# Kernel tuning notes

Hardware: AMD Instinct MI355X
Metric: run time of the kernel (lower is better)

Reference implementation:

```python
import jax, jax.numpy as jnp
import numpy as np

B, S, H, I, E, K = 2, 1024, 768, 1536, 8, 2
CAPACITY_FACTOR = 1.5
ROUTING_TEMP = 1.0
LB_WEIGHT = 0.001


def setup_inputs() -> dict:
    key = jax.random.key(0)
    k_x, k_g, k_w1, k_w3, k_w2 = jax.random.split(key, 5)
    std = 0.02
    return {
        "x": jax.random.normal(k_x, (B, S, H), dtype=jnp.float32),
        "w_gate": jax.random.normal(k_g, (H, E), dtype=jnp.float32) * 0.02,
        "w1": jax.random.normal(k_w1, (E, H, I), dtype=jnp.float32) * std,
        "w3": jax.random.normal(k_w3, (E, H, I), dtype=jnp.float32) * std,
        "w2": jax.random.normal(k_w2, (E, I, H), dtype=jnp.float32) * (std / np.sqrt(2 * 12)),
    }


def _moe_forward(x, w_gate, w1, w3, w2):
    Bb, Ss, Hh = x.shape
    T = Bb * Ss
    xf = x.reshape(T, Hh)

    # --- routing ---
    gate_logits = (xf @ w_gate) / ROUTING_TEMP          # [T, E]
    gate_probs = jax.nn.softmax(gate_logits, axis=-1)   # [T, E]
    topk_probs, topk_idx = jax.lax.top_k(gate_probs, K)  # [T, K]
    topk_probs = topk_probs / (topk_probs.sum(-1, keepdims=True) + 1e-8)

    # --- capacity dropping (per-k slot, token order, like the torch loop) ---
    capacity = max(8, int((T * K // E) * CAPACITY_FACTOR))
    onehot = (topk_idx[:, :, None] == jnp.arange(E)[None, None, :])  # [T, K, E] bool
    ranks = jnp.cumsum(onehot.astype(jnp.int32), axis=0)             # position of token in expert queue
    keep = onehot & (ranks <= capacity)                               # [T, K, E]

    # combine weight per (token, expert): sum over k of kept, clamped routing prob
    w_clamped = jnp.clip(topk_probs, 1e-8, 10.0)                      # [T, K]
    combine = jnp.einsum("tk,tke->te", w_clamped, keep.astype(xf.dtype))  # [T, E]

    # --- dense per-expert SwiGLU (reference form of masked dispatch) ---
    g = jnp.einsum("th,ehi->tei", xf, w1)   # [T, E, I]
    u = jnp.einsum("th,ehi->tei", xf, w3)   # [T, E, I]
    h = jax.nn.silu(g) * u                    # [T, E, I]
    y = jnp.einsum("tei,eih->teh", h, w2)   # [T, E, H]
    out = jnp.einsum("te,teh->th", combine, y).reshape(Bb, Ss, Hh)

    # --- load balancing loss ---
    expert_counts = keep.sum(axis=(0, 1)).astype(jnp.float32)         # [E]
    dropped = (onehot.sum() - keep.sum()).astype(jnp.float32)
    expert_usage = jax.lax.stop_gradient(expert_counts) / float(max(T * K, 1))
    gate_importance = gate_probs.mean(axis=0)                          # [E]
    aux = jnp.sum(expert_usage * gate_importance) * E
    aux = aux + jnp.where(dropped > 0, dropped / float(max(T, 1)) * 0.1, 0.0)
    aux = jnp.minimum(aux, 1.0) * LB_WEIGHT
    return out, aux


def reference(x, w_gate, w1, w3, w2):
    return _moe_forward(x, w_gate, w1, w3, w2)
```

## Files before the change

kernel.cpp:

```cpp
#include <hip/hip_runtime.h>
#include <math.h>

#define T_TOK 2048
#define HD 768
#define ID 1536
#define NE 8
#define CAP 768
#define TK 4096
#define RT 12
#define NB1 24
#define KC1 24
#define NB2 12
#define KC2 48
#define W2BLK 576

typedef __bf16 bf16_t;
typedef __bf16 bf16x8 __attribute__((ext_vector_type(8)));
typedef __bf16 bf16x4 __attribute__((ext_vector_type(4)));
typedef float floatx4 __attribute__((ext_vector_type(4)));

__device__ __forceinline__ void gld16(const bf16_t* g, bf16_t* l) {
  __builtin_amdgcn_global_load_lds(
      (__attribute__((address_space(1))) void*)(g),
      (__attribute__((address_space(3))) void*)(l),
      16, 0, 0);
}

__device__ __forceinline__ void repack_unit256(const float* __restrict__ src,
                                               bf16_t* __restrict__ dst, int C,
                                               int kc0, int tid) {
  int n = tid >> 2, p4 = tid & 3;
  int c8 = p4 ^ ((n >> 1) & 3);
  const float* sp0 = src + n + (size_t)(kc0 * 32 + c8 * 8) * C;
  bf16_t* dp = dst + (size_t)kc0 * 2048 + tid * 8;
#pragma unroll 2
  for (int t = 0; t < 8; ++t) {
    const float* sp = sp0 + (size_t)t * 32 * C;
    float v[8];
#pragma unroll
    for (int j = 0; j < 8; ++j) v[j] = sp[(size_t)j * C];
    bf16x8 o;
#pragma unroll
    for (int j = 0; j < 8; ++j) o[j] = (bf16_t)v[j];
    *(bf16x8*)(dp + t * 2048) = o;
  }
}

__device__ __forceinline__ void repack_unit1024(const float* __restrict__ src,
                                                bf16_t* __restrict__ dst, int C,
                                                int kc0, int tid1024) {
  int tid = tid1024 & 255;
  int tq = tid1024 >> 8;
  int n = tid >> 2, p4 = tid & 3;
  int c8 = p4 ^ ((n >> 1) & 3);
  const float* sp0 = src + n + (size_t)(kc0 * 32 + c8 * 8) * C;
  bf16_t* dp = dst + (size_t)kc0 * 2048 + tid * 8;
#pragma unroll
  for (int tt = 0; tt < 2; ++tt) {
    int t = tq * 2 + tt;
    const float* sp = sp0 + (size_t)t * 32 * C;
    float v[8];
#pragma unroll
    for (int j = 0; j < 8; ++j) v[j] = sp[(size_t)j * C];
    bf16x8 o;
#pragma unroll
    for (int j = 0; j < 8; ++j) o[j] = (bf16_t)v[j];
    *(bf16x8*)(dp + t * 2048) = o;
  }
}

__global__ void k_route(const float* __restrict__ x, const float* __restrict__ wg,
                        bf16_t* __restrict__ xbf, int2* __restrict__ idx2,
                        float2* __restrict__ wc2, float* __restrict__ probs8) {
  int b = blockIdx.x;
  int tid = threadIdx.x;
  int t = b * 4 + (tid >> 6);
  int lane = tid & 63;
  const float* xr = x + (size_t)t * HD;
  int off = lane * 12;
  float4 a = *(const float4*)(xr + off);
  float4 bv = *(const float4*)(xr + off + 4);
  float4 c = *(const float4*)(xr + off + 8);
  float xv[12] = {a.x, a.y, a.z, a.w, bv.x, bv.y, bv.z, bv.w, c.x, c.y, c.z, c.w};
  bf16x4 s0, s1, s2;
#pragma unroll
  for (int j = 0; j < 4; ++j) { s0[j] = (bf16_t)xv[j]; s1[j] = (bf16_t)xv[4 + j]; s2[j] = (bf16_t)xv[8 + j]; }
  bf16_t* xo = xbf + (size_t)t * HD + off;
  *(bf16x4*)xo = s0; *(bf16x4*)(xo + 4) = s1; *(bf16x4*)(xo + 8) = s2;

  float acc[8] = {0, 0, 0, 0, 0, 0, 0, 0};
#pragma unroll
  for (int jj = 0; jj < 12; ++jj) {
    const float4* wr = (const float4*)(wg + (size_t)(off + jj) * 8);
    float4 w0 = wr[0], w1v = wr[1];
    float v = xv[jj];
    acc[0] += v * w0.x; acc[1] += v * w0.y; acc[2] += v * w0.z; acc[3] += v * w0.w;
    acc[4] += v * w1v.x; acc[5] += v * w1v.y; acc[6] += v * w1v.z; acc[7] += v * w1v.w;
  }
#pragma unroll
  for (int e = 0; e < 8; ++e) {
    float v = acc[e];
    for (int s = 1; s < 64; s <<= 1) v += __shfl_xor(v, s, 64);
    acc[e] = v;
  }
  float mx = acc[0];
#pragma unroll
  for (int e = 1; e < 8; ++e) mx = fmaxf(mx, acc[e]);
  float p[8], sum = 0.f;
#pragma unroll
  for (int e = 0; e < 8; ++e) { p[e] = __expf(acc[e] - mx); sum += p[e]; }
#pragma unroll
  for (int e = 0; e < 8; ++e) p[e] /= sum;
  if (lane == 0) {
    float4 P0 = make_float4(p[0], p[1], p[2], p[3]);
    float4 P1 = make_float4(p[4], p[5], p[6], p[7]);
    *(float4*)&probs8[t * 8] = P0;
    *(float4*)&probs8[t * 8 + 4] = P1;
    int e0 = 0;
#pragma unroll
    for (int e = 1; e < 8; ++e) if (p[e] > p[e0]) e0 = e;
    int e1 = (e0 == 0) ? 1 : 0;
#pragma unroll
    for (int e = 0; e < 8; ++e) if (e != e0 && p[e] > p[e1]) e1 = e;
    float denom = p[e0] + p[e1] + 1e-8f;
    float w0c = fminf(fmaxf(p[e0] / denom, 1e-8f), 10.f);
    float w1c = fminf(fmaxf(p[e1] / denom, 1e-8f), 10.f);
    idx2[t] = make_int2(e0, e1);
    wc2[t] = make_float2(w0c, w1c);
  }
}

__global__ void k_scan(const int2* __restrict__ idx2, const float2* __restrict__ wc2,
                       const float* __restrict__ probs8,
                       const float* __restrict__ w1, const float* __restrict__ w3,
                       bf16_t* __restrict__ w1b, bf16_t* __restrict__ w3b,
                       int* __restrict__ tok_of_row, int2* __restrict__ rows2,
                       int2* __restrict__ cnt_start, float* __restrict__ aux_out) {
  if (blockIdx.x > 0) {
    int rb = blockIdx.x - 1;
    int m = rb >= 576;
    int r3 = m ? rb - 576 : rb;
    int pan = r3 / 3;
    int kc0 = (r3 - pan * 3) * 8;
    int e = pan & 7, nb = pan >> 3;
    const float* src = (m ? w3 : w1) + (size_t)e * HD * ID + nb * 64;
    bf16_t* dst = (m ? w3b : w1b) + (size_t)(e * NB1 + nb) * (KC1 * 2048);
    repack_unit1024(src, dst, ID, kc0, threadIdx.x);
    return;
  }
  __shared__ int2 sIdx[2048];
  __shared__ int sTot[16];
  __shared__ int sPos[8];
  __shared__ float sImp[16][8];
  int tid = threadIdx.x;
  sIdx[tid] = idx2[tid]; sIdx[tid + 1024] = idx2[tid + 1024];
  rows2[tid] = make_int2(-1, -1); rows2[tid + 1024] = make_int2(-1, -1);
  const float4* pp = (const float4*)probs8;
  float4 u0 = pp[tid * 4], u1 = pp[tid * 4 + 1], u2 = pp[tid * 4 + 2], u3 = pp[tid * 4 + 3];
  float im[8] = {u0.x + u2.x, u0.y + u2.y, u0.z + u2.z, u0.w + u2.w,
                 u1.x + u3.x, u1.y + u3.y, u1.z + u3.z, u1.w + u3.w};
#pragma unroll
  for (int e = 0; e < 8; ++e) {
    float v = im[e];
    for (int d = 1; d < 64; d <<= 1) v += __shfl_xor(v, d, 64);
    im[e] = v;
  }
  int w = tid >> 6, lane = tid & 63;
  if (lane == 0) {
#pragma unroll
    for (int e = 0; e < 8; ++e) sImp[w][e] = im[e];
  }
  __syncthreads();
  int s = w >> 3, e = w & 7;
  int t0 = lane * 32;
  int cnt = 0;
  for (int j = 0; j < 32; ++j) {
    int2 p = sIdx[t0 + j];
    cnt += ((s ? p.y : p.x) == e) ? 1 : 0;
  }
  int incl = cnt;
  for (int d = 1; d < 64; d <<= 1) {
    int v = __shfl_up(incl, d, 64);
    if (lane >= d) incl += v;
  }
  int excl = incl - cnt;
  if (lane == 63) sTot[w] = incl;
  __syncthreads();
  if (tid == 0) {
    int run = 0; float a = 0.f;
    for (int ee = 0; ee < 8; ++ee) {
      float impv = 0.f;
      for (int ww = 0; ww < 16; ++ww) impv += sImp[ww][ee];
      int k = min(sTot[ee], CAP) + min(sTot[8 + ee], CAP);
      sPos[ee] = run;
      cnt_start[ee] = make_int2(run, k);
      a += ((float)k / (float)TK) * (impv / (float)T_TOK);
      run += k;
    }
    a *= (float)NE;
    int dropped = TK - run;
    if (dropped > 0) a += (float)dropped / (float)T_TOK * 0.1f;
    aux_out[0] = fminf(a, 1.f) * 0.001f;
  }
  __syncthreads();
  int rank = excl;
  for (int j = 0; j < 32; ++j) {
    int t = t0 + j;
    int2 p = sIdx[t];
    int ex = s ? p.y : p.x;
    if (ex == e) {
      rank++;
      if (rank <= CAP) {
        int pos = atomicAdd(&sPos[e], 1);
        tok_of_row[pos] = t;
        ((int*)rows2)[2 * t + s] = pos;
      }
    }
  }
}

__global__ __launch_bounds__(256, 4)
void k_gemm1(const bf16_t* __restrict__ xbf, const bf16_t* __restrict__ w1b,
             const bf16_t* __restrict__ w3b, const float* __restrict__ w2,
             bf16_t* __restrict__ w2b, const int* __restrict__ tok_of_row,
             const int2* __restrict__ cnt_start, bf16_t* __restrict__ h_ws) {
  if (blockIdx.x < W2BLK) {
    int q = blockIdx.x;
    int pan = q / 6;
    int kc0 = (q - pan * 6) * 8;
    int e = pan & 7, nb = pan >> 3;
    const float* src = w2 + (size_t)e * ID * HD + nb * 64;
    bf16_t* dst = w2b + (size_t)(e * NB2 + nb) * (KC2 * 2048);
    repack_unit256(src, dst, HD, kc0, threadIdx.x);
    return;
  }
  int bx = blockIdx.x - W2BLK;
  int e = bx & 7;
  int t = bx >> 3;
  int nb = t / RT, rt = t - nb * RT;
  int2 cs = cnt_start[e];
  int nrows = cs.y - rt * 128;
  if (nrows <= 0) return;
  if (nrows > 128) nrows = 128;
  int grow0 = cs.x + rt * 128;

  __shared__ __attribute__((aligned(16))) bf16_t Abuf[128 * 32];
  __shared__ __attribute__((aligned(16))) bf16_t B1buf[64 * 32];
  __shared__ __attribute__((aligned(16))) bf16_t B3buf[64 * 32];

  int tid = threadIdx.x;
  int lane = tid & 63, wv = tid >> 6;
  int wm = wv & 1, wn = wv >> 1;
  int lr = lane & 15, q = lane >> 4;
  int rdc = (q ^ ((lane >> 1) & 3)) * 8;
  int srow = lane >> 2;
  int gch = ((lane & 3) ^ ((lane >> 3) & 3)) * 8;

  int ra = wv * 32 + srow;
  int tokA0 = tok_of_row[grow0 + min(ra, nrows - 1)];
  int tokA1 = tok_of_row[grow0 + min(ra + 16, nrows - 1)];
  const bf16_t* gA0 = xbf + (size_t)tokA0 * HD + gch;
  const bf16_t* gA1 = xbf + (size_t)tokA1 * HD + gch;
  const bf16_t* p1 = w1b + (size_t)((e * NB1 + nb) * KC1) * 2048 + tid * 8;
  const bf16_t* p3 = w3b + (size_t)((e * NB1 + nb) * KC1) * 2048 + tid * 8;
  bf16_t* lA0 = &Abuf[(wv * 32) * 32];
  bf16_t* lA1 = &Abuf[(wv * 32 + 16) * 32];
  bf16_t* lB1 = &B1buf[wv * 512];
  bf16_t* lB3 = &B3buf[wv * 512];

  floatx4 accg[4][2] = {};
  floatx4 accu[4][2] = {};

  for (int kk = 0; kk < KC1; ++kk) {
    __syncthreads();
    gld16(gA0, lA0); gld16(gA1, lA1);
    gld16(p1, lB1); gld16(p3, lB3);
    gA0 += 32; gA1 += 32; p1 += 2048; p3 += 2048;
    __syncthreads();
    bf16x8 af[4], b1f[2], b3f[2];
#pragma unroll
    for (int i = 0; i < 4; ++i) af[i] = *(const bf16x8*)&Abuf[(wm * 64 + i * 16 + lr) * 32 + rdc];
#pragma unroll
    for (int i = 0; i < 2; ++i) b1f[i] = *(const bf16x8*)&B1buf[(wn * 32 + i * 16 + lr) * 32 + rdc];
#pragma unroll
    for (int i = 0; i < 2; ++i) b3f[i] = *(const bf16x8*)&B3buf[(wn * 32 + i * 16 + lr) * 32 + rdc];
#pragma unroll
    for (int i = 0; i < 4; ++i)
#pragma unroll
      for (int jj = 0; jj < 2; ++jj) {
        accg[i][jj] = __builtin_amdgcn_mfma_f32_16x16x32_bf16(af[i], b1f[jj], accg[i][jj], 0, 0, 0);
        accu[i][jj] = __builtin_amdgcn_mfma_f32_16x16x32_bf16(af[i], b3f[jj], accu[i][jj], 0, 0, 0);
      }
  }
#pragma unroll
  for (int i = 0; i < 4; ++i)
#pragma unroll
    for (int r = 0; r < 4; ++r) {
      int rl = wm * 64 + i * 16 + q * 4 + r;
      if (rl < nrows) {
        size_t rb = (size_t)(grow0 + rl) * ID + nb * 64 + wn * 32 + lr;
#pragma unroll
        for (int jj = 0; jj < 2; ++jj) {
          float gg = accg[i][jj][r], uu = accu[i][jj][r];
          float sg = gg / (1.f + __expf(-gg));
          h_ws[rb + jj * 16] = (bf16_t)(sg * uu);
        }
      }
    }
}

__global__ __launch_bounds__(256, 4)
void k_gemm2(const bf16_t* __restrict__ h_ws, const bf16_t* __restrict__ w2b,
             const int2* __restrict__ cnt_start, float* __restrict__ y) {
  int e = blockIdx.x & 7;
  int t = blockIdx.x >> 3;
  int nb = t / RT, rt = t - nb * RT;
  int2 cs = cnt_start[e];
  int nrows = cs.y - rt * 128;
  if (nrows <= 0) return;
  if (nrows > 128) nrows = 128;
  int grow0 = cs.x + rt * 128;

  __shared__ __attribute__((aligned(16))) bf16_t Abuf[128 * 32];
  __shared__ __attribute__((aligned(16))) bf16_t Bbuf[64 * 32];

  int tid = threadIdx.x;
  int lane = tid & 63, wv = tid >> 6;
  int wm = wv & 1, wn = wv >> 1;
  int lr = lane & 15, q = lane >> 4;
  int rdc = (q ^ ((lane >> 1) & 3)) * 8;
  int srow = lane >> 2;
  int gch = ((lane & 3) ^ ((lane >> 3) & 3)) * 8;

  int ra = wv * 32 + srow;
  const bf16_t* gA0 = h_ws + (size_t)(grow0 + min(ra, nrows - 1)) * ID + gch;
  const bf16_t* gA1 = h_ws + (size_t)(grow0 + min(ra + 16, nrows - 1)) * ID + gch;
  const bf16_t* pB = w2b + (size_t)((e * NB2 + nb) * KC2) * 2048 + tid * 8;
  bf16_t* lA0 = &Abuf[(wv * 32) * 32];
  bf16_t* lA1 = &Abuf[(wv * 32 + 16) * 32];
  bf16_t* lB = &Bbuf[wv * 512];

  floatx4 acc[4][2] = {};

  for (int kk = 0; kk < KC2; ++kk) {
    __syncthreads();
    gld16(gA0, lA0); gld16(gA1, lA1);
    gld16(pB, lB);
    gA0 += 32; gA1 += 32; pB += 2048;
    __syncthreads();
    bf16x8 af[4], bfr[2];
#pragma unroll
    for (int i = 0; i < 4; ++i) af[i] = *(const bf16x8*)&Abuf[(wm * 64 + i * 16 + lr) * 32 + rdc];
#pragma unroll
    for (int i = 0; i < 2; ++i) bfr[i] = *(const bf16x8*)&Bbuf[(wn * 32 + i * 16 + lr) * 32 + rdc];
#pragma unroll
    for (int i = 0; i < 4; ++i)
#pragma unroll
      for (int jj = 0; jj < 2; ++jj)
        acc[i][jj] = __builtin_amdgcn_mfma_f32_16x16x32_bf16(af[i], bfr[jj], acc[i][jj], 0, 0, 0);
  }
#pragma unroll
  for (int i = 0; i < 4; ++i)
#pragma unroll
    for (int r = 0; r < 4; ++r) {
      int rl = wm * 64 + i * 16 + q * 4 + r;
      if (rl < nrows) {
        size_t ob = (size_t)(grow0 + rl) * HD + nb * 64 + wn * 32 + lr;
#pragma unroll
        for (int jj = 0; jj < 2; ++jj)
          y[ob + jj * 16] = acc[i][jj][r];
      }
    }
}

__global__ void k_comb(const float* __restrict__ y, const int2* __restrict__ rows2,
                       const float2* __restrict__ wc2, float* __restrict__ out) {
  int tid = threadIdx.x;
  int t = blockIdx.x * 4 + (tid >> 6);
  int lane = tid & 63;
  int2 r = rows2[t];
  float2 w = wc2[t];
  int off = lane * 12;
  floatx4 o0 = {0.f, 0.f, 0.f, 0.f}, o1 = o0, o2 = o0;
  if (r.x >= 0) {
    const float* yr = y + (size_t)r.x * HD + off;
    floatx4 a = *(const floatx4*)(yr);
    floatx4 b = *(const floatx4*)(yr + 4);
    floatx4 c = *(const floatx4*)(yr + 8);
    o0 += w.x * a; o1 += w.x * b; o2 += w.x * c;
  }
  if (r.y >= 0) {
    const float* yr = y + (size_t)r.y * HD + off;
    floatx4 a = *(const floatx4*)(yr);
    floatx4 b = *(const floatx4*)(yr + 4);
    floatx4 c = *(const floatx4*)(yr + 8);
    o0 += w.y * a; o1 += w.y * b; o2 += w.y * c;
  }
  float* op = out + (size_t)t * HD + off;
  *(floatx4*)(op) = o0;
  *(floatx4*)(op + 4) = o1;
  *(floatx4*)(op + 8) = o2;
}

extern "C" void kernel_launch(void* const* d_in, const int* in_sizes, int n_in,
                              void* d_out, int out_size, void* d_ws, size_t ws_size,
                              hipStream_t stream) {
  const float* x  = (const float*)d_in[0];
  const float* wg = (const float*)d_in[1];
  const float* w1 = (const float*)d_in[2];
  const float* w3 = (const float*)d_in[3];
  const float* w2 = (const float*)d_in[4];
  float* out = (float*)d_out;

  char* ws = (char*)d_ws;
  bf16_t* xbf  = (bf16_t*)(ws + 0);
  bf16_t* w1b  = (bf16_t*)(ws + 3145728);
  bf16_t* w3b  = (bf16_t*)(ws + 22020096);
  bf16_t* w2b  = (bf16_t*)(ws + 40894464);
  bf16_t* h_ws = (bf16_t*)(ws + 59768832);
  float*  probs8     = (float*)(ws + 72351744);
  int2*   idx2       = (int2*)(ws + 72417280);
  float2* wc2        = (float2*)(ws + 72433664);
  int*    tok_of_row = (int*)(ws + 72450048);
  int2*   rows2      = (int2*)(ws + 72466432);
  int2*   cnt_start  = (int2*)(ws + 72482816);
  float*  y_ws = (float*)(ws + 3145728);

  float* aux_out = out + (size_t)T_TOK * HD;

  k_route<<<512, 256, 0, stream>>>(x, wg, xbf, idx2, wc2, probs8);
  k_scan<<<1 + 1152, 1024, 0, stream>>>(idx2, wc2, probs8, w1, w3, w1b, w3b,
                                        tok_of_row, rows2, cnt_start, aux_out);
  k_gemm1<<<W2BLK + 8 * NB1 * RT, 256, 0, stream>>>(xbf, w1b, w3b, w2, w2b,
                                                    tok_of_row, cnt_start, h_ws);
  k_gemm2<<<8 * NB2 * RT, 256, 0, stream>>>(h_ws, w2b, cnt_start, y_ws);
  k_comb<<<512, 256, 0, stream>>>(y_ws, rows2, wc2, out);
}
```

Before: 235.5 us.

## Double-buffer LDS tiles in both expert GEMM kernels to overlap loads with MFMA

Both grouped GEMM kernels now keep two LDS buffers for the A and B tiles. The next K-chunk is prefetched with global_load_lds while MFMAs run on the current chunk, which also cuts the barriers per iteration from two to one. The aim is to hide global-to-LDS load latency behind compute. In exchange, LDS use per block doubles, which could limit occupancy. The overlap also depends on the compiler not inserting a full vmcnt wait before the LDS reads.

After: 238.4 us. About the same (+1.2%).

```diff
diff --git a/kernel.cpp b/kernel.cpp
--- a/kernel.cpp
+++ b/kernel.cpp
@@ -244,9 +244,9 @@
   if (nrows > 128) nrows = 128;
   int grow0 = cs.x + rt * 128;
 
-  __shared__ __attribute__((aligned(16))) bf16_t Abuf[128 * 32];
-  __shared__ __attribute__((aligned(16))) bf16_t B1buf[64 * 32];
-  __shared__ __attribute__((aligned(16))) bf16_t B3buf[64 * 32];
+  __shared__ __attribute__((aligned(16))) bf16_t Abuf[2][128 * 32];
+  __shared__ __attribute__((aligned(16))) bf16_t B1buf[2][64 * 32];
+  __shared__ __attribute__((aligned(16))) bf16_t B3buf[2][64 * 32];
 
   int tid = threadIdx.x;
   int lane = tid & 63, wv = tid >> 6;
@@ -263,27 +263,30 @@
   const bf16_t* gA1 = xbf + (size_t)tokA1 * HD + gch;
   const bf16_t* p1 = w1b + (size_t)((e * NB1 + nb) * KC1) * 2048 + tid * 8;
   const bf16_t* p3 = w3b + (size_t)((e * NB1 + nb) * KC1) * 2048 + tid * 8;
-  bf16_t* lA0 = &Abuf[(wv * 32) * 32];
-  bf16_t* lA1 = &Abuf[(wv * 32 + 16) * 32];
-  bf16_t* lB1 = &B1buf[wv * 512];
-  bf16_t* lB3 = &B3buf[wv * 512];
 
   floatx4 accg[4][2] = {};
   floatx4 accu[4][2] = {};
 
+  gld16(gA0, &Abuf[0][wv * 1024]); gld16(gA1, &Abuf[0][wv * 1024 + 512]);
+  gld16(p1, &B1buf[0][wv * 512]); gld16(p3, &B3buf[0][wv * 512]);
+  gA0 += 32; gA1 += 32; p1 += 2048; p3 += 2048;
+  __syncthreads();
+
   for (int kk = 0; kk < KC1; ++kk) {
-    __syncthreads();
-    gld16(gA0, lA0); gld16(gA1, lA1);
-    gld16(p1, lB1); gld16(p3, lB3);
-    gA0 += 32; gA1 += 32; p1 += 2048; p3 += 2048;
-    __syncthreads();
+    int cur = kk & 1;
+    if (kk + 1 < KC1) {
+      int nxt = cur ^ 1;
+      gld16(gA0, &Abuf[nxt][wv * 1024]); gld16(gA1, &Abuf[nxt][wv * 1024 + 512]);
+      gld16(p1, &B1buf[nxt][wv * 512]); gld16(p3, &B3buf[nxt][wv * 512]);
+      gA0 += 32; gA1 += 32; p1 += 2048; p3 += 2048;
+    }
     bf16x8 af[4], b1f[2], b3f[2];
 #pragma unroll
-    for (int i = 0; i < 4; ++i) af[i] = *(const bf16x8*)&Abuf[(wm * 64 + i * 16 + lr) * 32 + rdc];
-#pragma unroll
-    for (int i = 0; i < 2; ++i) b1f[i] = *(const bf16x8*)&B1buf[(wn * 32 + i * 16 + lr) * 32 + rdc];
-#pragma unroll
-    for (int i = 0; i < 2; ++i) b3f[i] = *(const bf16x8*)&B3buf[(wn * 32 + i * 16 + lr) * 32 + rdc];
+    for (int i = 0; i < 4; ++i) af[i] = *(const bf16x8*)&Abuf[cur][(wm * 64 + i * 16 + lr) * 32 + rdc];
+#pragma unroll
+    for (int i = 0; i < 2; ++i) b1f[i] = *(const bf16x8*)&B1buf[cur][(wn * 32 + i * 16 + lr) * 32 + rdc];
+#pragma unroll
+    for (int i = 0; i < 2; ++i) b3f[i] = *(const bf16x8*)&B3buf[cur][(wn * 32 + i * 16 + lr) * 32 + rdc];
 #pragma unroll
     for (int i = 0; i < 4; ++i)
 #pragma unroll
@@ -291,6 +294,7 @@
         accg[i][jj] = __builtin_amdgcn_mfma_f32_16x16x32_bf16(af[i], b1f[jj], accg[i][jj], 0, 0, 0);
         accu[i][jj] = __builtin_amdgcn_mfma_f32_16x16x32_bf16(af[i], b3f[jj], accu[i][jj], 0, 0, 0);
       }
+    if (kk + 1 < KC1) __syncthreads();
   }
 #pragma unroll
   for (int i = 0; i < 4; ++i)
@@ -321,8 +325,8 @@
   if (nrows > 128) nrows = 128;
   int grow0 = cs.x + rt * 128;
 
-  __shared__ __attribute__((aligned(16))) bf16_t Abuf[128 * 32];
-  __shared__ __attribute__((aligned(16))) bf16_t Bbuf[64 * 32];
+  __shared__ __attribute__((aligned(16))) bf16_t Abuf[2][128 * 32];
+  __shared__ __attribute__((aligned(16))) bf16_t Bbuf[2][64 * 32];
 
   int tid = threadIdx.x;
   int lane = tid & 63, wv = tid >> 6;
@@ -336,28 +340,33 @@
   const bf16_t* gA0 = h_ws + (size_t)(grow0 + min(ra, nrows - 1)) * ID + gch;
   const bf16_t* gA1 = h_ws + (size_t)(grow0 + min(ra + 16, nrows - 1)) * ID + gch;
   const bf16_t* pB = w2b + (size_t)((e * NB2 + nb) * KC2) * 2048 + tid * 8;
-  bf16_t* lA0 = &Abuf[(wv * 32) * 32];
-  bf16_t* lA1 = &Abuf[(wv * 32 + 16) * 32];
-  bf16_t* lB = &Bbuf[wv * 512];
 
   floatx4 acc[4][2] = {};
 
+  gld16(gA0, &Abuf[0][wv * 1024]); gld16(gA1, &Abuf[0][wv * 1024 + 512]);
+  gld16(pB, &Bbuf[0][wv * 512]);
+  gA0 += 32; gA1 += 32; pB += 2048;
+  __syncthreads();
+
   for (int kk = 0; kk < KC2; ++kk) {
-    __syncthreads();
-    gld16(gA0, lA0); gld16(gA1, lA1);
-    gld16(pB, lB);
-    gA0 += 32; gA1 += 32; pB += 2048;
-    __syncthreads();
+    int cur = kk & 1;
+    if (kk + 1 < KC2) {
+      int nxt = cur ^ 1;
+      gld16(gA0, &Abuf[nxt][wv * 1024]); gld16(gA1, &Abuf[nxt][wv * 1024 + 512]);
+      gld16(pB, &Bbuf[nxt][wv * 512]);
+      gA0 += 32; gA1 += 32; pB += 2048;
+    }
     bf16x8 af[4], bfr[2];
 #pragma unroll
-    for (int i = 0; i < 4; ++i) af[i] = *(const bf16x8*)&Abuf[(wm * 64 + i * 16 + lr) * 32 + rdc];
-#pragma unroll
-    for (int i = 0; i < 2; ++i) bfr[i] = *(const bf16x8*)&Bbuf[(wn * 32 + i * 16 + lr) * 32 + rdc];
+    for (int i = 0; i < 4; ++i) af[i] = *(const bf16x8*)&Abuf[cur][(wm * 64 + i * 16 + lr) * 32 + rdc];
+#pragma unroll
+    for (int i = 0; i < 2; ++i) bfr[i] = *(const bf16x8*)&Bbuf[cur][(wn * 32 + i * 16 + lr) * 32 + rdc];
 #pragma unroll
     for (int i = 0; i < 4; ++i)
 #pragma unroll
       for (int jj = 0; jj < 2; ++jj)
         acc[i][jj] = __builtin_amdgcn_mfma_f32_16x16x32_bf16(af[i], bfr[jj], acc[i][jj], 0, 0, 0);
+    if (kk + 1 < KC2) __syncthreads();
   }
 #pragma unroll
   for (int i = 0; i < 4; ++i)
```

## Fuse fp32-to-bf16 weight conversion into GEMM B-tile loads, drop repack passes

Applied to the files above, without the earlier changes.

Removes the separate passes that converted w1, w3 and w2 from fp32 to a swizzled bf16 layout in the workspace. Each GEMM block now reads fp32 weights straight from global memory, converts them in registers and writes them into LDS inside the K loop. This saves the write and re-read of about 56MB of bf16 weights and the extra repack blocks. In exchange, each weight tile is re-read in fp32 by every row-tile block (12 per expert), and the loads are strided, synchronous register loads rather than async global-to-LDS loads. gemm1's launch bound drops to 3 blocks per SM.

Measured after the change: 349.9 us. +48.6%, slower.

```diff
diff --git a/kernel.cpp b/kernel.cpp
--- a/kernel.cpp
+++ b/kernel.cpp
@@ -12,7 +12,6 @@
 #define KC1 24
 #define NB2 12
 #define KC2 48
-#define W2BLK 576
 
 typedef __bf16 bf16_t;
 typedef __bf16 bf16x8 __attribute__((ext_vector_type(8)));
@@ -24,49 +23,6 @@
       (__attribute__((address_space(1))) void*)(g),
       (__attribute__((address_space(3))) void*)(l),
       16, 0, 0);
-}
-
-__device__ __forceinline__ void repack_unit256(const float* __restrict__ src,
-                                               bf16_t* __restrict__ dst, int C,
-                                               int kc0, int tid) {
-  int n = tid >> 2, p4 = tid & 3;
-  int c8 = p4 ^ ((n >> 1) & 3);
-  const float* sp0 = src + n + (size_t)(kc0 * 32 + c8 * 8) * C;
-  bf16_t* dp = dst + (size_t)kc0 * 2048 + tid * 8;
-#pragma unroll 2
-  for (int t = 0; t < 8; ++t) {
-    const float* sp = sp0 + (size_t)t * 32 * C;
-    float v[8];
-#pragma unroll
-    for (int j = 0; j < 8; ++j) v[j] = sp[(size_t)j * C];
-    bf16x8 o;
-#pragma unroll
-    for (int j = 0; j < 8; ++j) o[j] = (bf16_t)v[j];
-    *(bf16x8*)(dp + t * 2048) = o;
-  }
-}
-
-__device__ __forceinline__ void repack_unit1024(const float* __restrict__ src,
-                                                bf16_t* __restrict__ dst, int C,
-                                                int kc0, int tid1024) {
-  int tid = tid1024 & 255;
-  int tq = tid1024 >> 8;
-  int n = tid >> 2, p4 = tid & 3;
-  int c8 = p4 ^ ((n >> 1) & 3);
-  const float* sp0 = src + n + (size_t)(kc0 * 32 + c8 * 8) * C;
-  bf16_t* dp = dst + (size_t)kc0 * 2048 + tid * 8;
-#pragma unroll
-  for (int tt = 0; tt < 2; ++tt) {
-    int t = tq * 2 + tt;
-    const float* sp = sp0 + (size_t)t * 32 * C;
-    float v[8];
-#pragma unroll
-    for (int j = 0; j < 8; ++j) v[j] = sp[(size_t)j * C];
-    bf16x8 o;
-#pragma unroll
-    for (int j = 0; j < 8; ++j) o[j] = (bf16_t)v[j];
-    *(bf16x8*)(dp + t * 2048) = o;
-  }
 }
 
 __global__ void k_route(const float* __restrict__ x, const float* __restrict__ wg,
@@ -132,22 +88,8 @@
 
 __global__ void k_scan(const int2* __restrict__ idx2, const float2* __restrict__ wc2,
                        const float* __restrict__ probs8,
-                       const float* __restrict__ w1, const float* __restrict__ w3,
-                       bf16_t* __restrict__ w1b, bf16_t* __restrict__ w3b,
                        int* __restrict__ tok_of_row, int2* __restrict__ rows2,
                        int2* __restrict__ cnt_start, float* __restrict__ aux_out) {
-  if (blockIdx.x > 0) {
-    int rb = blockIdx.x - 1;
-    int m = rb >= 576;
-    int r3 = m ? rb - 576 : rb;
-    int pan = r3 / 3;
-    int kc0 = (r3 - pan * 3) * 8;
-    int e = pan & 7, nb = pan >> 3;
-    const float* src = (m ? w3 : w1) + (size_t)e * HD * ID + nb * 64;
-    bf16_t* dst = (m ? w3b : w1b) + (size_t)(e * NB1 + nb) * (KC1 * 2048);
-    repack_unit1024(src, dst, ID, kc0, threadIdx.x);
-    return;
-  }
   __shared__ int2 sIdx[2048];
   __shared__ int sTot[16];
   __shared__ int sPos[8];
@@ -219,24 +161,12 @@
   }
 }
 
-__global__ __launch_bounds__(256, 4)
-void k_gemm1(const bf16_t* __restrict__ xbf, const bf16_t* __restrict__ w1b,
-             const bf16_t* __restrict__ w3b, const float* __restrict__ w2,
-             bf16_t* __restrict__ w2b, const int* __restrict__ tok_of_row,
+__global__ __launch_bounds__(256, 3)
+void k_gemm1(const bf16_t* __restrict__ xbf, const float* __restrict__ w1,
+             const float* __restrict__ w3, const int* __restrict__ tok_of_row,
              const int2* __restrict__ cnt_start, bf16_t* __restrict__ h_ws) {
-  if (blockIdx.x < W2BLK) {
-    int q = blockIdx.x;
-    int pan = q / 6;
-    int kc0 = (q - pan * 6) * 8;
-    int e = pan & 7, nb = pan >> 3;
-    const float* src = w2 + (size_t)e * ID * HD + nb * 64;
-    bf16_t* dst = w2b + (size_t)(e * NB2 + nb) * (KC2 * 2048);
-    repack_unit256(src, dst, HD, kc0, threadIdx.x);
-    return;
-  }
-  int bx = blockIdx.x - W2BLK;
-  int e = bx & 7;
-  int t = bx >> 3;
+  int e = blockIdx.x & 7;
+  int t = blockIdx.x >> 3;
   int nb = t / RT, rt = t - nb * RT;
   int2 cs = cnt_start[e];
   int nrows = cs.y - rt * 128;
@@ -261,12 +191,15 @@
   int tokA1 = tok_of_row[grow0 + min(ra + 16, nrows - 1)];
   const bf16_t* gA0 = xbf + (size_t)tokA0 * HD + gch;
   const bf16_t* gA1 = xbf + (size_t)tokA1 * HD + gch;
-  const bf16_t* p1 = w1b + (size_t)((e * NB1 + nb) * KC1) * 2048 + tid * 8;
-  const bf16_t* p3 = w3b + (size_t)((e * NB1 + nb) * KC1) * 2048 + tid * 8;
   bf16_t* lA0 = &Abuf[(wv * 32) * 32];
   bf16_t* lA1 = &Abuf[(wv * 32 + 16) * 32];
-  bf16_t* lB1 = &B1buf[wv * 512];
-  bf16_t* lB3 = &B3buf[wv * 512];
+
+  int n = tid >> 2, p4 = tid & 3;
+  int c8 = p4 ^ ((n >> 1) & 3);
+  const float* s1 = w1 + (size_t)e * HD * ID + nb * 64 + n + (size_t)(c8 * 8) * ID;
+  const float* s3 = w3 + (size_t)e * HD * ID + nb * 64 + n + (size_t)(c8 * 8) * ID;
+  bf16_t* d1 = &B1buf[tid * 8];
+  bf16_t* d3 = &B3buf[tid * 8];
 
   floatx4 accg[4][2] = {};
   floatx4 accu[4][2] = {};
@@ -274,8 +207,21 @@
   for (int kk = 0; kk < KC1; ++kk) {
     __syncthreads();
     gld16(gA0, lA0); gld16(gA1, lA1);
-    gld16(p1, lB1); gld16(p3, lB3);
-    gA0 += 32; gA1 += 32; p1 += 2048; p3 += 2048;
+    gA0 += 32; gA1 += 32;
+    {
+      const float* sp1 = s1 + (size_t)kk * 32 * ID;
+      const float* sp3 = s3 + (size_t)kk * 32 * ID;
+      float v1[8], v3[8];
+#pragma unroll
+      for (int j = 0; j < 8; ++j) v1[j] = sp1[(size_t)j * ID];
+#pragma unroll
+      for (int j = 0; j < 8; ++j) v3[j] = sp3[(size_t)j * ID];
+      bf16x8 o1, o3;
+#pragma unroll
+      for (int j = 0; j < 8; ++j) { o1[j] = (bf16_t)v1[j]; o3[j] = (bf16_t)v3[j]; }
+      *(bf16x8*)d1 = o1;
+      *(bf16x8*)d3 = o3;
+    }
     __syncthreads();
     bf16x8 af[4], b1f[2], b3f[2];
 #pragma unroll
@@ -310,7 +256,7 @@
 }
 
 __global__ __launch_bounds__(256, 4)
-void k_gemm2(const bf16_t* __restrict__ h_ws, const bf16_t* __restrict__ w2b,
+void k_gemm2(const bf16_t* __restrict__ h_ws, const float* __restrict__ w2,
              const int2* __restrict__ cnt_start, float* __restrict__ y) {
   int e = blockIdx.x & 7;
   int t = blockIdx.x >> 3;
@@ -335,18 +281,30 @@
   int ra = wv * 32 + srow;
   const bf16_t* gA0 = h_ws + (size_t)(grow0 + min(ra, nrows - 1)) * ID + gch;
   const bf16_t* gA1 = h_ws + (size_t)(grow0 + min(ra + 16, nrows - 1)) * ID + gch;
-  const bf16_t* pB = w2b + (size_t)((e * NB2 + nb) * KC2) * 2048 + tid * 8;
   bf16_t* lA0 = &Abuf[(wv * 32) * 32];
   bf16_t* lA1 = &Abuf[(wv * 32 + 16) * 32];
-  bf16_t* lB = &Bbuf[wv * 512];
+
+  int n = tid >> 2, p4 = tid & 3;
+  int c8 = p4 ^ ((n >> 1) & 3);
+  const float* s2 = w2 + (size_t)e * ID * HD + nb * 64 + n + (size_t)(c8 * 8) * HD;
+  bf16_t* d2 = &Bbuf[tid * 8];
 
   floatx4 acc[4][2] = {};
 
   for (int kk = 0; kk < KC2; ++kk) {
     __syncthreads();
     gld16(gA0, lA0); gld16(gA1, lA1);
-    gld16(pB, lB);
-    gA0 += 32; gA1 += 32; pB += 2048;
+    gA0 += 32; gA1 += 32;
+    {
+      const float* sp = s2 + (size_t)kk * 32 * HD;
+      float v[8];
+#pragma unroll
+      for (int j = 0; j < 8; ++j) v[j] = sp[(size_t)j * HD];
+      bf16x8 o;
+#pragma unroll
+      for (int j = 0; j < 8; ++j) o[j] = (bf16_t)v[j];
+      *(bf16x8*)d2 = o;
+    }
     __syncthreads();
     bf16x8 af[4], bfr[2];
 #pragma unroll
@@ -414,25 +372,22 @@
 
   char* ws = (char*)d_ws;
   bf16_t* xbf  = (bf16_t*)(ws + 0);
-  bf16_t* w1b  = (bf16_t*)(ws + 3145728);
-  bf16_t* w3b  = (bf16_t*)(ws + 22020096);
-  bf16_t* w2b  = (bf16_t*)(ws + 40894464);
-  bf16_t* h_ws = (bf16_t*)(ws + 59768832);
-  float*  probs8     = (float*)(ws + 72351744);
-  int2*   idx2       = (int2*)(ws + 72417280);
-  float2* wc2        = (float2*)(ws + 72433664);
-  int*    tok_of_row = (int*)(ws + 72450048);
-  int2*   rows2      = (int2*)(ws + 72466432);
-  int2*   cnt_start  = (int2*)(ws + 72482816);
-  float*  y_ws = (float*)(ws + 3145728);
+  bf16_t* h_ws = (bf16_t*)(ws + 3145728);
+  float*  y_ws = (float*)(ws + 15728640);
+  float*  probs8     = (float*)(ws + 28311552);
+  int2*   idx2       = (int2*)(ws + 28377088);
+  float2* wc2        = (float2*)(ws + 28393472);
+  int*    tok_of_row = (int*)(ws + 28409856);
+  int2*   rows2      = (int2*)(ws + 28426240);
+  int2*   cnt_start  = (int2*)(ws + 28459008);
 
   float* aux_out = out + (size_t)T_TOK * HD;
 
   k_route<<<512, 256, 0, stream>>>(x, wg, xbf, idx2, wc2, probs8);
-  k_scan<<<1 + 1152, 1024, 0, stream>>>(idx2, wc2, probs8, w1, w3, w1b, w3b,
-                                        tok_of_row, rows2, cnt_start, aux_out);
-  k_gemm1<<<W2BLK + 8 * NB1 * RT, 256, 0, stream>>>(xbf, w1b, w3b, w2, w2b,
-                                                    tok_of_row, cnt_start, h_ws);
-  k_gemm2<<<8 * NB2 * RT, 256, 0, stream>>>(h_ws, w2b, cnt_start, y_ws);
+  k_scan<<<1, 1024, 0, stream>>>(idx2, wc2, probs8, tok_of_row, rows2,
+                                 cnt_start, aux_out);
+  k_gemm1<<<8 * NB1 * RT, 256, 0, stream>>>(xbf, w1, w3, tok_of_row,
+                                            cnt_start, h_ws);
+  k_gemm2<<<8 * NB2 * RT, 256, 0, stream>>>(h_ws, w2, cnt_start, y_ws);
   k_comb<<<512, 256, 0, stream>>>(y_ws, rows2, wc2, out);
 }
```

## Move all weight repacks into routing kernel and deepen GEMM K-steps per barrier

Applied to the files above, without the earlier changes.

All fp32-to-bf16 weight repacks (w1, w3, w2) now run as extra blocks of the routing kernel. This takes them out of the single-block scan kernel and out of the first GEMM, so the scan runs alone and GEMM1 launches only compute blocks. GEMM1 now loads two K-chunks per barrier pair and GEMM2 loads four, which halves or quarters the barrier count but raises LDS use; GEMM2's launch bound drops to 3 blocks per CU. The repack blocks now use 256 threads each instead of the 1024-thread variant, and w2's repack now has to finish before GEMM1 rather than overlapping with it.

Result: slower. 253.7 us (+7.8%).

```diff
diff --git a/kernel.cpp b/kernel.cpp
--- a/kernel.cpp
+++ b/kernel.cpp
@@ -12,7 +12,6 @@
 #define KC1 24
 #define NB2 12
 #define KC2 48
-#define W2BLK 576
 
 typedef __bf16 bf16_t;
 typedef __bf16 bf16x8 __attribute__((ext_vector_type(8)));
@@ -46,34 +45,39 @@
   }
 }
 
-__device__ __forceinline__ void repack_unit1024(const float* __restrict__ src,
-                                                bf16_t* __restrict__ dst, int C,
-                                                int kc0, int tid1024) {
-  int tid = tid1024 & 255;
-  int tq = tid1024 >> 8;
-  int n = tid >> 2, p4 = tid & 3;
-  int c8 = p4 ^ ((n >> 1) & 3);
-  const float* sp0 = src + n + (size_t)(kc0 * 32 + c8 * 8) * C;
-  bf16_t* dp = dst + (size_t)kc0 * 2048 + tid * 8;
-#pragma unroll
-  for (int tt = 0; tt < 2; ++tt) {
-    int t = tq * 2 + tt;
-    const float* sp = sp0 + (size_t)t * 32 * C;
-    float v[8];
-#pragma unroll
-    for (int j = 0; j < 8; ++j) v[j] = sp[(size_t)j * C];
-    bf16x8 o;
-#pragma unroll
-    for (int j = 0; j < 8; ++j) o[j] = (bf16_t)v[j];
-    *(bf16x8*)(dp + t * 2048) = o;
-  }
-}
-
 __global__ void k_route(const float* __restrict__ x, const float* __restrict__ wg,
-                        bf16_t* __restrict__ xbf, int2* __restrict__ idx2,
-                        float2* __restrict__ wc2, float* __restrict__ probs8) {
+                        const float* __restrict__ w1, const float* __restrict__ w3,
+                        const float* __restrict__ w2,
+                        bf16_t* __restrict__ xbf, bf16_t* __restrict__ w1b,
+                        bf16_t* __restrict__ w3b, bf16_t* __restrict__ w2b,
+                        int2* __restrict__ idx2, float2* __restrict__ wc2,
+                        float* __restrict__ probs8) {
   int b = blockIdx.x;
   int tid = threadIdx.x;
+  if (b >= 512) {
+    int rb = b - 512;
+    const float* src; bf16_t* dst; int C; int kc0;
+    if (rb < 1152) {
+      int m = rb >= 576;
+      int r3 = m ? rb - 576 : rb;
+      int pan = r3 / 3;
+      kc0 = (r3 - pan * 3) * 8;
+      int e = pan & 7, nb = pan >> 3;
+      src = (m ? w3 : w1) + (size_t)e * HD * ID + nb * 64;
+      dst = (m ? w3b : w1b) + (size_t)(e * NB1 + nb) * (KC1 * 2048);
+      C = ID;
+    } else {
+      int q = rb - 1152;
+      int pan = q / 6;
+      kc0 = (q - pan * 6) * 8;
+      int e = pan & 7, nb = pan >> 3;
+      src = w2 + (size_t)e * ID * HD + nb * 64;
+      dst = w2b + (size_t)(e * NB2 + nb) * (KC2 * 2048);
+      C = HD;
+    }
+    repack_unit256(src, dst, C, kc0, tid);
+    return;
+  }
   int t = b * 4 + (tid >> 6);
   int lane = tid & 63;
   const float* xr = x + (size_t)t * HD;
@@ -132,22 +136,8 @@
 
 __global__ void k_scan(const int2* __restrict__ idx2, const float2* __restrict__ wc2,
                        const float* __restrict__ probs8,
-                       const float* __restrict__ w1, const float* __restrict__ w3,
-                       bf16_t* __restrict__ w1b, bf16_t* __restrict__ w3b,
                        int* __restrict__ tok_of_row, int2* __restrict__ rows2,
                        int2* __restrict__ cnt_start, float* __restrict__ aux_out) {
-  if (blockIdx.x > 0) {
-    int rb = blockIdx.x - 1;
-    int m = rb >= 576;
-    int r3 = m ? rb - 576 : rb;
-    int pan = r3 / 3;
-    int kc0 = (r3 - pan * 3) * 8;
-    int e = pan & 7, nb = pan >> 3;
-    const float* src = (m ? w3 : w1) + (size_t)e * HD * ID + nb * 64;
-    bf16_t* dst = (m ? w3b : w1b) + (size_t)(e * NB1 + nb) * (KC1 * 2048);
-    repack_unit1024(src, dst, ID, kc0, threadIdx.x);
-    return;
-  }
   __shared__ int2 sIdx[2048];
   __shared__ int sTot[16];
   __shared__ int sPos[8];
@@ -221,22 +211,10 @@
 
 __global__ __launch_bounds__(256, 4)
 void k_gemm1(const bf16_t* __restrict__ xbf, const bf16_t* __restrict__ w1b,
-             const bf16_t* __restrict__ w3b, const float* __restrict__ w2,
-             bf16_t* __restrict__ w2b, const int* __restrict__ tok_of_row,
+             const bf16_t* __restrict__ w3b, const int* __restrict__ tok_of_row,
              const int2* __restrict__ cnt_start, bf16_t* __restrict__ h_ws) {
-  if (blockIdx.x < W2BLK) {
-    int q = blockIdx.x;
-    int pan = q / 6;
-    int kc0 = (q - pan * 6) * 8;
-    int e = pan & 7, nb = pan >> 3;
-    const float* src = w2 + (size_t)e * ID * HD + nb * 64;
-    bf16_t* dst = w2b + (size_t)(e * NB2 + nb) * (KC2 * 2048);
-    repack_unit256(src, dst, HD, kc0, threadIdx.x);
-    return;
-  }
-  int bx = blockIdx.x - W2BLK;
-  int e = bx & 7;
-  int t = bx >> 3;
+  int e = blockIdx.x & 7;
+  int t = blockIdx.x >> 3;
   int nb = t / RT, rt = t - nb * RT;
   int2 cs = cnt_start[e];
   int nrows = cs.y - rt * 128;
@@ -244,9 +222,9 @@
   if (nrows > 128) nrows = 128;
   int grow0 = cs.x + rt * 128;
 
-  __shared__ __attribute__((aligned(16))) bf16_t Abuf[128 * 32];
-  __shared__ __attribute__((aligned(16))) bf16_t B1buf[64 * 32];
-  __shared__ __attribute__((aligned(16))) bf16_t B3buf[64 * 32];
+  __shared__ __attribute__((aligned(16))) bf16_t Abuf[2][128 * 32];
+  __shared__ __attribute__((aligned(16))) bf16_t B1buf[2][64 * 32];
+  __shared__ __attribute__((aligned(16))) bf16_t B3buf[2][64 * 32];
 
   int tid = threadIdx.x;
   int lane = tid & 63, wv = tid >> 6;
@@ -263,34 +241,43 @@
   const bf16_t* gA1 = xbf + (size_t)tokA1 * HD + gch;
   const bf16_t* p1 = w1b + (size_t)((e * NB1 + nb) * KC1) * 2048 + tid * 8;
   const bf16_t* p3 = w3b + (size_t)((e * NB1 + nb) * KC1) * 2048 + tid * 8;
-  bf16_t* lA0 = &Abuf[(wv * 32) * 32];
-  bf16_t* lA1 = &Abuf[(wv * 32 + 16) * 32];
-  bf16_t* lB1 = &B1buf[wv * 512];
-  bf16_t* lB3 = &B3buf[wv * 512];
+  bf16_t* lA0_0 = &Abuf[0][(wv * 32) * 32];
+  bf16_t* lA1_0 = &Abuf[0][(wv * 32 + 16) * 32];
+  bf16_t* lA0_1 = &Abuf[1][(wv * 32) * 32];
+  bf16_t* lA1_1 = &Abuf[1][(wv * 32 + 16) * 32];
+  bf16_t* lB1_0 = &B1buf[0][wv * 512];
+  bf16_t* lB3_0 = &B3buf[0][wv * 512];
+  bf16_t* lB1_1 = &B1buf[1][wv * 512];
+  bf16_t* lB3_1 = &B3buf[1][wv * 512];
 
   floatx4 accg[4][2] = {};
   floatx4 accu[4][2] = {};
 
-  for (int kk = 0; kk < KC1; ++kk) {
+  for (int g = 0; g < KC1 / 2; ++g) {
     __syncthreads();
-    gld16(gA0, lA0); gld16(gA1, lA1);
-    gld16(p1, lB1); gld16(p3, lB3);
-    gA0 += 32; gA1 += 32; p1 += 2048; p3 += 2048;
+    gld16(gA0, lA0_0); gld16(gA1, lA1_0);
+    gld16(p1, lB1_0); gld16(p3, lB3_0);
+    gld16(gA0 + 32, lA0_1); gld16(gA1 + 32, lA1_1);
+    gld16(p1 + 2048, lB1_1); gld16(p3 + 2048, lB3_1);
+    gA0 += 64; gA1 += 64; p1 += 4096; p3 += 4096;
     __syncthreads();
-    bf16x8 af[4], b1f[2], b3f[2];
-#pragma unroll
-    for (int i = 0; i < 4; ++i) af[i] = *(const bf16x8*)&Abuf[(wm * 64 + i * 16 + lr) * 32 + rdc];
-#pragma unroll
-    for (int i = 0; i < 2; ++i) b1f[i] = *(const bf16x8*)&B1buf[(wn * 32 + i * 16 + lr) * 32 + rdc];
-#pragma unroll
-    for (int i = 0; i < 2; ++i) b3f[i] = *(const bf16x8*)&B3buf[(wn * 32 + i * 16 + lr) * 32 + rdc];
-#pragma unroll
-    for (int i = 0; i < 4; ++i)
-#pragma unroll
-      for (int jj = 0; jj < 2; ++jj) {
-        accg[i][jj] = __builtin_amdgcn_mfma_f32_16x16x32_bf16(af[i], b1f[jj], accg[i][jj], 0, 0, 0);
-        accu[i][jj] = __builtin_amdgcn_mfma_f32_16x16x32_bf16(af[i], b3f[jj], accu[i][jj], 0, 0, 0);
-      }
+#pragma unroll
+    for (int s = 0; s < 2; ++s) {
+      bf16x8 af[4], b1f[2], b3f[2];
+#pragma unroll
+      for (int i = 0; i < 4; ++i) af[i] = *(const bf16x8*)&Abuf[s][(wm * 64 + i * 16 + lr) * 32 + rdc];
+#pragma unroll
+      for (int i = 0; i < 2; ++i) b1f[i] = *(const bf16x8*)&B1buf[s][(wn * 32 + i * 16 + lr) * 32 + rdc];
+#pragma unroll
+      for (int i = 0; i < 2; ++i) b3f[i] = *(const bf16x8*)&B3buf[s][(wn * 32 + i * 16 + lr) * 32 + rdc];
+#pragma unroll
+      for (int i = 0; i < 4; ++i)
+#pragma unroll
+        for (int jj = 0; jj < 2; ++jj) {
+          accg[i][jj] = __builtin_amdgcn_mfma_f32_16x16x32_bf16(af[i], b1f[jj], accg[i][jj], 0, 0, 0);
+          accu[i][jj] = __builtin_amdgcn_mfma_f32_16x16x32_bf16(af[i], b3f[jj], accu[i][jj], 0, 0, 0);
+        }
+    }
   }
 #pragma unroll
   for (int i = 0; i < 4; ++i)
@@ -309,7 +296,7 @@
     }
 }
 
-__global__ __launch_bounds__(256, 4)
+__global__ __launch_bounds__(256, 3)
 void k_gemm2(const bf16_t* __restrict__ h_ws, const bf16_t* __restrict__ w2b,
              const int2* __restrict__ cnt_start, float* __restrict__ y) {
   int e = blockIdx.x & 7;
@@ -321,8 +308,8 @@
   if (nrows > 128) nrows = 128;
   int grow0 = cs.x + rt * 128;
 
-  __shared__ __attribute__((aligned(16))) bf16_t Abuf[128 * 32];
-  __shared__ __attribute__((aligned(16))) bf16_t Bbuf[64 * 32];
+  __shared__ __attribute__((aligned(16))) bf16_t Abuf[4][128 * 32];
+  __shared__ __attribute__((aligned(16))) bf16_t Bbuf[4][64 * 32];
 
   int tid = threadIdx.x;
   int lane = tid & 63, wv = tid >> 6;
@@ -336,28 +323,32 @@
   const bf16_t* gA0 = h_ws + (size_t)(grow0 + min(ra, nrows - 1)) * ID + gch;
   const bf16_t* gA1 = h_ws + (size_t)(grow0 + min(ra + 16, nrows - 1)) * ID + gch;
   const bf16_t* pB = w2b + (size_t)((e * NB2 + nb) * KC2) * 2048 + tid * 8;
-  bf16_t* lA0 = &Abuf[(wv * 32) * 32];
-  bf16_t* lA1 = &Abuf[(wv * 32 + 16) * 32];
-  bf16_t* lB = &Bbuf[wv * 512];
 
   floatx4 acc[4][2] = {};
 
-  for (int kk = 0; kk < KC2; ++kk) {
+  for (int g = 0; g < KC2 / 4; ++g) {
     __syncthreads();
-    gld16(gA0, lA0); gld16(gA1, lA1);
-    gld16(pB, lB);
-    gA0 += 32; gA1 += 32; pB += 2048;
+#pragma unroll
+    for (int s = 0; s < 4; ++s) {
+      gld16(gA0 + s * 32, &Abuf[s][(wv * 32) * 32]);
+      gld16(gA1 + s * 32, &Abuf[s][(wv * 32 + 16) * 32]);
+      gld16(pB + s * 2048, &Bbuf[s][wv * 512]);
+    }
+    gA0 += 128; gA1 += 128; pB += 8192;
     __syncthreads();
-    bf16x8 af[4], bfr[2];
-#pragma unroll
-    for (int i = 0; i < 4; ++i) af[i] = *(const bf16x8*)&Abuf[(wm * 64 + i * 16 + lr) * 32 + rdc];
-#pragma unroll
-    for (int i = 0; i < 2; ++i) bfr[i] = *(const bf16x8*)&Bbuf[(wn * 32 + i * 16 + lr) * 32 + rdc];
-#pragma unroll
-    for (int i = 0; i < 4; ++i)
-#pragma unroll
-      for (int jj = 0; jj < 2; ++jj)
-        acc[i][jj] = __builtin_amdgcn_mfma_f32_16x16x32_bf16(af[i], bfr[jj], acc[i][jj], 0, 0, 0);
+#pragma unroll
+    for (int s = 0; s < 4; ++s) {
+      bf16x8 af[4], bfr[2];
+#pragma unroll
+      for (int i = 0; i < 4; ++i) af[i] = *(const bf16x8*)&Abuf[s][(wm * 64 + i * 16 + lr) * 32 + rdc];
+#pragma unroll
+      for (int i = 0; i < 2; ++i) bfr[i] = *(const bf16x8*)&Bbuf[s][(wn * 32 + i * 16 + lr) * 32 + rdc];
+#pragma unroll
+      for (int i = 0; i < 4; ++i)
+#pragma unroll
+        for (int jj = 0; jj < 2; ++jj)
+          acc[i][jj] = __builtin_amdgcn_mfma_f32_16x16x32_bf16(af[i], bfr[jj], acc[i][jj], 0, 0, 0);
+    }
   }
 #pragma unroll
   for (int i = 0; i < 4; ++i)
@@ -428,11 +419,12 @@
 
   float* aux_out = out + (size_t)T_TOK * HD;
 
-  k_route<<<512, 256, 0, stream>>>(x, wg, xbf, idx2, wc2, probs8);
-  k_scan<<<1 + 1152, 1024, 0, stream>>>(idx2, wc2, probs8, w1, w3, w1b, w3b,
-                                        tok_of_row, rows2, cnt_start, aux_out);
-  k_gemm1<<<W2BLK + 8 * NB1 * RT, 256, 0, stream>>>(xbf, w1b, w3b, w2, w2b,
-                                                    tok_of_row, cnt_start, h_ws);
+  k_route<<<512 + 1728, 256, 0, stream>>>(x, wg, w1, w3, w2, xbf, w1b, w3b, w2b,
+                                          idx2, wc2, probs8);
+  k_scan<<<1, 1024, 0, stream>>>(idx2, wc2, probs8, tok_of_row, rows2,
+                                 cnt_start, aux_out);
+  k_gemm1<<<8 * NB1 * RT, 256, 0, stream>>>(xbf, w1b, w3b, tok_of_row,
+                                            cnt_start, h_ws);
   k_gemm2<<<8 * NB2 * RT, 256, 0, stream>>>(h_ws, w2b, cnt_start, y_ws);
   k_comb<<<512, 256, 0, stream>>>(y_ws, rows2, wc2, out);
 }
```
